# Kernel tuning notes

Hardware: AMD Instinct MI355X
Metric: run time of the kernel (lower is better)

Reference implementation:

```python
import jax, jax.numpy as jnp
import numpy as np

KNN = 8
T = 0.07
EPS = 1e-7

def l2norm(x):
    return x / jnp.sqrt(jnp.sum(x * x, axis=1, keepdims=True))

def nce_softmax_loss(x):
    # CrossEntropyLoss with all labels == 0
    return jnp.mean(jax.nn.logsumexp(x, axis=1) - x[:, 0])

def knn_indices(logits, k):
    # cos_distance_softmax on a single 'sample' [N, C]
    soft = jax.nn.softmax(logits, axis=-1)                      # [N, C]
    w = jnp.linalg.norm(soft, axis=-1)                          # [N]
    sim = (soft @ soft.T) / jnp.clip(w[:, None] * w[None, :], EPS)
    dist = 1.0 - sim
    eye = jnp.eye(logits.shape[0], dtype=dist.dtype)
    dist = dist * (1.0 - eye) - eye                             # diag -> -1 so self is always picked
    _, nbr = jax.lax.top_k(-dist, k)                            # k smallest distances
    return nbr                                                   # [N, k]

def gnn_encode(h, nbr, W, b):
    # DGL TAGConv with k=1 on the knn graph. Edges are j->i for j in knn(i),
    # so every node has in-degree KNN and D^-1/2 A D^-1/2 h == mean over knn neighbors.
    agg = jnp.mean(h[nbr], axis=1)                              # [N, C]
    return l2norm(jnp.concatenate([h, agg], axis=1) @ W + b)

def setup_inputs():
    key = jax.random.key(0)
    ks = jax.random.split(key, 16)
    B, S_DIM, T_DIM, C, N_DATA, K, NCLS = 256, 1024, 2048, 128, 200000, 4096, 100
    stdv = 1.0 / np.sqrt(C / 3.0)
    return {
        "epoch": 1,
        "f_s": jax.random.normal(ks[0], (B, S_DIM), jnp.float32),
        "l_s": jax.random.normal(ks[1], (B, NCLS), jnp.float32),
        "f_t": jax.random.normal(ks[2], (B, T_DIM), jnp.float32),
        "l_t": jax.random.normal(ks[3], (B, NCLS), jnp.float32),
        "idx": jax.random.randint(ks[4], (B,), 0, N_DATA, jnp.int32),
        "contrast_idx": jax.random.randint(ks[5], (B, K), 0, N_DATA, jnp.int32),
        "W_es": jax.random.normal(ks[6], (C, S_DIM), jnp.float32) / np.sqrt(S_DIM),
        "b_es": jnp.zeros((C,), jnp.float32),
        "W_et": jax.random.normal(ks[7], (C, T_DIM), jnp.float32) / np.sqrt(T_DIM),
        "b_et": jnp.zeros((C,), jnp.float32),
        "W_gs": jax.random.normal(ks[8], (2 * C, C), jnp.float32) / np.sqrt(2 * C),
        "b_gs": jnp.zeros((C,), jnp.float32),
        "W_gt": jax.random.normal(ks[9], (2 * C, C), jnp.float32) / np.sqrt(2 * C),
        "b_gt": jnp.zeros((C,), jnp.float32),
        "memory_l": jax.random.uniform(ks[10], (N_DATA, C), jnp.float32, -stdv, stdv),
        "memory_ab": jax.random.uniform(ks[11], (N_DATA, C), jnp.float32, -stdv, stdv),
    }

def reference(epoch, f_s, l_s, f_t, l_t, idx, contrast_idx,
              W_es, b_es, W_et, b_et, W_gs, b_gs, W_gt, b_gt,
              memory_l, memory_ab):
    mem_l = jax.lax.stop_gradient(memory_l)
    mem_ab = jax.lax.stop_gradient(memory_ab)

    # Embed + L2 normalize
    f_es = l2norm(f_s @ W_es.T + b_es)                          # [B, C]
    f_et = l2norm(f_t @ W_et.T + b_et)                          # [B, C]

    # NCEAverage.forward: gather negatives from memory banks
    weight_t = mem_l[contrast_idx]                              # [B, K, C]
    weight_s = mem_ab[contrast_idx]                             # [B, K, C]
    # get_pos
    f_us = mem_l[idx]                                           # [B, C]
    f_ut = mem_ab[idx]                                          # [B, C]

    ls_pos = jnp.sum(f_ut * f_es, axis=1, keepdims=True)        # [B, 1]
    lt_pos = jnp.sum(f_us * f_et, axis=1, keepdims=True)
    ls_neg = jnp.einsum('bkc,bc->bk', weight_t, f_es)           # [B, K]
    lt_neg = jnp.einsum('bkc,bc->bk', weight_s, f_et)
    out_s = jnp.concatenate([ls_pos, ls_neg], axis=1) / T
    out_t = jnp.concatenate([lt_pos, lt_neg], axis=1) / T
    loss = nce_softmax_loss(out_s) + nce_softmax_loss(out_t)

    # GNN branch (batchSize >= knn)
    nbr_s = knn_indices(jax.lax.stop_gradient(l_s), KNN)
    f_gs = gnn_encode(f_es, nbr_s, W_gs, b_gs)                  # [B, C]
    nbr_t = knn_indices(jax.lax.stop_gradient(l_t), KNN)
    f_gt = gnn_encode(f_et, nbr_t, W_gt, b_gt)

    # get_smooth (fully detached, momentum 0.75)
    f_sgs = jax.lax.stop_gradient(l2norm(mem_l[idx] * 0.75 + f_gs * 0.25))
    f_sgt = jax.lax.stop_gradient(l2norm(mem_ab[idx] * 0.75 + f_gt * 0.25))

    gs_pos = jnp.sum(f_sgt * f_gs, axis=1, keepdims=True)
    gt_pos = jnp.sum(f_sgs * f_gt, axis=1, keepdims=True)
    gs_neg = jnp.einsum('bkc,bc->bk', weight_t, f_gs)
    gt_neg = jnp.einsum('bkc,bc->bk', weight_s, f_gt)
    out_gs = jnp.concatenate([gs_pos, gs_neg], axis=1) / T
    out_gt = jnp.concatenate([gt_pos, gt_neg], axis=1) / T
    loss_g = nce_softmax_loss(out_gs) + nce_softmax_loss(out_gt)

    # NOTE: contrast.update() is a no-grad buffer mutation with no effect on the
    # returned loss; omitted from the pure-functional reference.
    return loss + loss_g
```

## Files before the change

### kernel.cpp

```cpp
#include <hip/hip_runtime.h>
#include <math.h>

#define B 256
#define SDIM 1024
#define TDIM 2048
#define C 128
#define NCLS 100
#define KNEG 4096
#define KNN_K 8
#define NCHUNK 16
#define KC (KNEG / NCHUNK)
#define TINV (1.0f / 0.07f)

__global__ __launch_bounds__(256) void embed2_kernel(
    const float* __restrict__ Xs, const float* __restrict__ Ws,
    const float* __restrict__ bs, const float* __restrict__ Xt,
    const float* __restrict__ Wt, const float* __restrict__ bt,
    float* __restrict__ out_s, float* __restrict__ out_t) {
  const int which = blockIdx.y;
  const int S = which ? TDIM : SDIM;
  const float* __restrict__ X = which ? Xt : Xs;
  const float* __restrict__ W = which ? Wt : Ws;
  const float* __restrict__ bias = which ? bt : bs;
  float* __restrict__ out = which ? out_t : out_s;

  __shared__ float xrow[TDIM];
  __shared__ float ob[C];
  __shared__ float ssbuf[4];
  const int b = blockIdx.x;
  const int t = threadIdx.x;
  const int wave = t >> 6, lane = t & 63;

  const float4* xg = (const float4*)(X + (size_t)b * S);
  for (int i = t; i < S / 4; i += 256) ((float4*)xrow)[i] = xg[i];
  __syncthreads();

  const int nj = S / 256;
  for (int ci = 0; ci < 32; ++ci) {
    const int c = wave * 32 + ci;
    const float4* wrow = (const float4*)(W + (size_t)c * S);
    float acc = 0.f;
    for (int j = 0; j < nj; ++j) {
      float4 w4 = wrow[lane + 64 * j];
      float4 x4 = ((const float4*)xrow)[lane + 64 * j];
      acc += w4.x * x4.x + w4.y * x4.y + w4.z * x4.z + w4.w * x4.w;
    }
#pragma unroll
    for (int off = 32; off; off >>= 1) acc += __shfl_xor(acc, off, 64);
    if (lane == 0) ob[c] = acc + bias[c];
  }
  __syncthreads();

  const float v = (t < C) ? ob[t] : 0.f;
  float ss = v * v;
#pragma unroll
  for (int off = 32; off; off >>= 1) ss += __shfl_xor(ss, off, 64);
  if (lane == 0) ssbuf[wave] = ss;
  __syncthreads();
  const float tot = ssbuf[0] + ssbuf[1] + ssbuf[2] + ssbuf[3];
  if (t < C) out[(size_t)b * C + t] = v / sqrtf(tot);
}

__global__ __launch_bounds__(128) void knn_soft_kernel(
    const float* __restrict__ Ls, const float* __restrict__ Lt,
    float* __restrict__ soft_s, float* __restrict__ soft_t,
    float* __restrict__ wn_s, float* __restrict__ wn_t) {
  const int which = blockIdx.y;
  const float* L = which ? Lt : Ls;
  float* soft = which ? soft_t : soft_s;
  float* wn = which ? wn_t : wn_s;
  const int b = blockIdx.x;
  const int t = threadIdx.x;
  const int wave = t >> 6, lane = t & 63;
  __shared__ float r2[2];

  const float x = (t < NCLS) ? L[b * NCLS + t] : -INFINITY;
  float m = x;
#pragma unroll
  for (int off = 32; off; off >>= 1) m = fmaxf(m, __shfl_xor(m, off, 64));
  if (lane == 0) r2[wave] = m;
  __syncthreads();
  m = fmaxf(r2[0], r2[1]);
  __syncthreads();

  const float e = (t < NCLS) ? expf(x - m) : 0.f;
  float s = e;
#pragma unroll
  for (int off = 32; off; off >>= 1) s += __shfl_xor(s, off, 64);
  if (lane == 0) r2[wave] = s;
  __syncthreads();
  s = r2[0] + r2[1];
  __syncthreads();

  const float p = e / s;
  if (t < NCLS) soft[b * NCLS + t] = p;

  float q = p * p;
#pragma unroll
  for (int off = 32; off; off >>= 1) q += __shfl_xor(q, off, 64);
  if (lane == 0) r2[wave] = q;
  __syncthreads();
  if (t == 0) wn[b] = sqrtf(r2[0] + r2[1]);
}

__global__ __launch_bounds__(256) void knn_topk_kernel(
    const float* __restrict__ soft_s, const float* __restrict__ wn_s,
    int* __restrict__ nbr_s, const float* __restrict__ soft_t,
    const float* __restrict__ wn_t, int* __restrict__ nbr_t) {
  const int which = blockIdx.y;
  const float* __restrict__ soft = which ? soft_t : soft_s;
  const float* __restrict__ wn = which ? wn_t : wn_s;
  int* __restrict__ nbr = which ? nbr_t : nbr_s;

  const int i = blockIdx.x;
  const int j = threadIdx.x;
  __shared__ float si[NCLS];
  __shared__ float vals[B];
  __shared__ float rv[B];
  __shared__ int ri[B];

  if (j < NCLS) si[j] = soft[i * NCLS + j];
  __syncthreads();

  float dot = 0.f;
  for (int c = 0; c < NCLS; ++c) dot += si[c] * soft[j * NCLS + c];
  const float denom = fmaxf(wn[i] * wn[j], 1e-7f);
  vals[j] = (j == i) ? 1.0f : (dot / denom - 1.0f);
  __syncthreads();

  for (int r = 0; r < KNN_K; ++r) {
    rv[j] = vals[j];
    ri[j] = j;
    __syncthreads();
    for (int s = 128; s; s >>= 1) {
      if (j < s) {
        const float v2 = rv[j + s];
        const int i2 = ri[j + s];
        if (v2 > rv[j] || (v2 == rv[j] && i2 < ri[j])) { rv[j] = v2; ri[j] = i2; }
      }
      __syncthreads();
    }
    if (j == 0) {
      nbr[i * KNN_K + r] = ri[0];
      vals[ri[0]] = -INFINITY;
    }
    __syncthreads();
  }
}

__global__ __launch_bounds__(256) void gnn_pos_kernel(
    const float* __restrict__ f_es, const float* __restrict__ f_et,
    const int* __restrict__ nbr_s, const int* __restrict__ nbr_t,
    const float* __restrict__ W_gs, const float* __restrict__ b_gs,
    const float* __restrict__ W_gt, const float* __restrict__ b_gt,
    const float* __restrict__ mem_l, const float* __restrict__ mem_ab,
    const int* __restrict__ idx, float* __restrict__ f_gs_out,
    float* __restrict__ f_gt_out, float* __restrict__ pos) {
  const int b = blockIdx.x;
  const int t = threadIdx.x;
  const int half = t >> 7;
  const int c = t & 127;
  const int wave = t >> 6, lane = t & 63;

  const float* __restrict__ h = half ? f_et : f_es;
  const int* __restrict__ nbr = half ? nbr_t : nbr_s;
  const float* __restrict__ Wg = half ? W_gt : W_gs;
  const float* __restrict__ bg = half ? b_gt : b_gs;

  __shared__ float hcat[2][2 * C];
  __shared__ float gbuf[2][C];
  __shared__ float red[4];
  __shared__ float r26[2][6];

  float agg = 0.f;
#pragma unroll
  for (int j = 0; j < KNN_K; ++j)
    agg += h[(size_t)nbr[b * KNN_K + j] * C + c];
  hcat[half][c] = h[(size_t)b * C + c];
  hcat[half][C + c] = agg * (1.0f / KNN_K);
  __syncthreads();

  float acc = bg[c];
  for (int k = 0; k < 2 * C; ++k) acc += hcat[half][k] * Wg[k * C + c];

  float ss = acc * acc;
#pragma unroll
  for (int off = 32; off; off >>= 1) ss += __shfl_xor(ss, off, 64);
  if (lane == 0) red[wave] = ss;
  __syncthreads();
  const float g = acc / sqrtf(red[half * 2] + red[half * 2 + 1]);
  gbuf[half][c] = g;
  (half ? f_gt_out : f_gs_out)[(size_t)b * C + c] = g;
  __syncthreads();

  if (half == 0) {
    const int id = idx[b];
    const float ml = mem_l[(size_t)id * C + c];
    const float mab = mem_ab[(size_t)id * C + c];
    const float es = f_es[(size_t)b * C + c];
    const float et = f_et[(size_t)b * C + c];
    const float gs = gbuf[0][c];
    const float gt = gbuf[1][c];
    const float sgs = 0.75f * ml + 0.25f * gs;
    const float sgt = 0.75f * mab + 0.25f * gt;

    float v6[6] = {sgs * sgs, sgt * sgt, mab * es, ml * et, sgt * gs, sgs * gt};
#pragma unroll
    for (int q = 0; q < 6; ++q) {
      float v = v6[q];
#pragma unroll
      for (int off = 32; off; off >>= 1) v += __shfl_xor(v, off, 64);
      if (lane == 0) r26[wave][q] = v;
    }
  }
  __syncthreads();
  if (t == 0) {
    const float ss_gs = r26[0][0] + r26[1][0];
    const float ss_gt = r26[0][1] + r26[1][1];
    pos[0 * B + b] = r26[0][2] + r26[1][2];
    pos[1 * B + b] = r26[0][3] + r26[1][3];
    pos[2 * B + b] = (r26[0][4] + r26[1][4]) / sqrtf(ss_gt);
    pos[3 * B + b] = (r26[0][5] + r26[1][5]) / sqrtf(ss_gs);
  }
}

__global__ __launch_bounds__(256) void neg_partial_kernel(
    const float* __restrict__ mem_l, const float* __restrict__ mem_ab,
    const int* __restrict__ cidx, const float* __restrict__ f_es,
    const float* __restrict__ f_et, const float* __restrict__ f_gs,
    const float* __restrict__ f_gt, float* __restrict__ partial) {
  const int b = blockIdx.x;
  const int chunk = blockIdx.y;
  const int bank = blockIdx.z;
  const float* __restrict__ mem = bank ? mem_ab : mem_l;
  const float* __restrict__ f1 = bank ? f_et : f_es;
  const float* __restrict__ f2 = bank ? f_gt : f_gs;
  const int t = threadIdx.x;
  const int wave = t >> 6, lane = t & 63;
  const int grp = t >> 4;
  const int lig = t & 15;

  __shared__ int rows[KC];
  __shared__ float rbuf[4][2];

  rows[t] = cidx[(size_t)b * KNEG + chunk * KC + t];

  const float4 x1lo = ((const float4*)f1)[b * 32 + lig];
  const float4 x1hi = ((const float4*)f1)[b * 32 + lig + 16];
  const float4 x2lo = ((const float4*)f2)[b * 32 + lig];
  const float4 x2hi = ((const float4*)f2)[b * 32 + lig + 16];
  __syncthreads();

  float s1 = 0.f, s2 = 0.f;
#pragma unroll
  for (int it = 0; it < 16; ++it) {
    const int row = rows[grp * 16 + it];
    const float4* __restrict__ r = (const float4*)(mem + (size_t)row * C);
    const float4 vlo = r[lig];
    const float4 vhi = r[lig + 16];
    float a1 = vlo.x * x1lo.x + vlo.y * x1lo.y + vlo.z * x1lo.z + vlo.w * x1lo.w
             + vhi.x * x1hi.x + vhi.y * x1hi.y + vhi.z * x1hi.z + vhi.w * x1hi.w;
    float a2 = vlo.x * x2lo.x + vlo.y * x2lo.y + vlo.z * x2lo.z + vlo.w * x2lo.w
             + vhi.x * x2hi.x + vhi.y * x2hi.y + vhi.z * x2hi.z + vhi.w * x2hi.w;
#pragma unroll
    for (int off = 8; off; off >>= 1) {
      a1 += __shfl_xor(a1, off, 64);
      a2 += __shfl_xor(a2, off, 64);
    }
    s1 += __expf(a1 * TINV);
    s2 += __expf(a2 * TINV);
  }
  s1 += __shfl_xor(s1, 32, 64);
  s1 += __shfl_xor(s1, 16, 64);
  s2 += __shfl_xor(s2, 32, 64);
  s2 += __shfl_xor(s2, 16, 64);
  if (lane == 0) { rbuf[wave][0] = s1; rbuf[wave][1] = s2; }
  __syncthreads();
  if (t == 0) {
    const float v1 = rbuf[0][0] + rbuf[1][0] + rbuf[2][0] + rbuf[3][0];
    const float v2 = rbuf[0][1] + rbuf[1][1] + rbuf[2][1] + rbuf[3][1];
    partial[((size_t)bank * B + b) * NCHUNK + chunk] = v1;
    partial[((size_t)(bank + 2) * B + b) * NCHUNK + chunk] = v2;
  }
}

__global__ __launch_bounds__(256) void loss_kernel(
    const float* __restrict__ partial, const float* __restrict__ pos,
    float* __restrict__ out) {
  const int b = threadIdx.x;
  const int wave = b >> 6, lane = b & 63;
  __shared__ float rb[4];
  float contrib = 0.f;
#pragma unroll
  for (int l = 0; l < 4; ++l) {
    const float p = pos[l * B + b] * TINV;
    float s = expf(p);
    for (int ch = 0; ch < NCHUNK; ++ch)
      s += partial[((size_t)l * B + b) * NCHUNK + ch];
    contrib += logf(s) - p;
  }
#pragma unroll
  for (int off = 32; off; off >>= 1) contrib += __shfl_xor(contrib, off, 64);
  if (lane == 0) rb[wave] = contrib;
  __syncthreads();
  if (b == 0) out[0] = (rb[0] + rb[1] + rb[2] + rb[3]) * (1.0f / B);
}

extern "C" void kernel_launch(void* const* d_in, const int* in_sizes, int n_in,
                              void* d_out, int out_size, void* d_ws,
                              size_t ws_size, hipStream_t stream) {
  const float* f_s = (const float*)d_in[1];
  const float* l_s = (const float*)d_in[2];
  const float* f_t = (const float*)d_in[3];
  const float* l_t = (const float*)d_in[4];
  const int* idx = (const int*)d_in[5];
  const int* cidx = (const int*)d_in[6];
  const float* W_es = (const float*)d_in[7];
  const float* b_es = (const float*)d_in[8];
  const float* W_et = (const float*)d_in[9];
  const float* b_et = (const float*)d_in[10];
  const float* W_gs = (const float*)d_in[11];
  const float* b_gs = (const float*)d_in[12];
  const float* W_gt = (const float*)d_in[13];
  const float* b_gt = (const float*)d_in[14];
  const float* mem_l = (const float*)d_in[15];
  const float* mem_ab = (const float*)d_in[16];

  char* w = (char*)d_ws;
  float* ws_f_es = (float*)w;    w += B * C * sizeof(float);
  float* ws_f_et = (float*)w;    w += B * C * sizeof(float);
  float* ws_f_gs = (float*)w;    w += B * C * sizeof(float);
  float* ws_f_gt = (float*)w;    w += B * C * sizeof(float);
  float* ws_soft_s = (float*)w;  w += B * NCLS * sizeof(float);
  float* ws_soft_t = (float*)w;  w += B * NCLS * sizeof(float);
  float* ws_wn_s = (float*)w;    w += B * sizeof(float);
  float* ws_wn_t = (float*)w;    w += B * sizeof(float);
  int* ws_nbr_s = (int*)w;       w += B * KNN_K * sizeof(int);
  int* ws_nbr_t = (int*)w;       w += B * KNN_K * sizeof(int);
  float* ws_pos = (float*)w;     w += 4 * B * sizeof(float);
  float* ws_partial = (float*)w; w += 4 * B * NCHUNK * sizeof(float);

  embed2_kernel<<<dim3(B, 2), 256, 0, stream>>>(f_s, W_es, b_es, f_t, W_et,
                                                b_et, ws_f_es, ws_f_et);

  knn_soft_kernel<<<dim3(B, 2), 128, 0, stream>>>(l_s, l_t, ws_soft_s,
                                                  ws_soft_t, ws_wn_s, ws_wn_t);

  knn_topk_kernel<<<dim3(B, 2), 256, 0, stream>>>(ws_soft_s, ws_wn_s, ws_nbr_s,
                                                  ws_soft_t, ws_wn_t, ws_nbr_t);

  gnn_pos_kernel<<<B, 256, 0, stream>>>(ws_f_es, ws_f_et, ws_nbr_s, ws_nbr_t,
                                        W_gs, b_gs, W_gt, b_gt, mem_l, mem_ab,
                                        idx, ws_f_gs, ws_f_gt, ws_pos);

  neg_partial_kernel<<<dim3(B, NCHUNK, 2), 256, 0, stream>>>(
      mem_l, mem_ab, cidx, ws_f_es, ws_f_et, ws_f_gs, ws_f_gt, ws_partial);

  loss_kernel<<<1, 256, 0, stream>>>(ws_partial, ws_pos, (float*)d_out);
}
```

Baseline: 435.4 us.

## Batch four rows per embed block, wave-level top-k, DPP reductions, prefetch negatives

The embed kernel now handles four batch rows per block, so each W row load feeds four dot products. Cross-lane sums use DPP-based reductions. The knn top-k replaces the shared-memory tree reduction, which needed many barriers, with a single-wave shuffle argmax over four values per lane. The negative-scoring kernel software-pipelines the gathered memory-bank rows two at a time. The embed change cuts the grid to 128 blocks and raises shared memory to 32KB, which may reduce occupancy and parallelism.

```diff
diff --git a/kernel.cpp b/kernel.cpp
--- a/kernel.cpp
+++ b/kernel.cpp
@@ -11,6 +11,28 @@
 #define NCHUNK 16
 #define KC (KNEG / NCHUNK)
 #define TINV (1.0f / 0.07f)
+
+template <int CTRL>
+__device__ __forceinline__ float dpp_add(float v) {
+  const int x = __builtin_amdgcn_update_dpp(0, __float_as_int(v), CTRL, 0xF, 0xF, true);
+  return v + __int_as_float(x);
+}
+__device__ __forceinline__ float sum16(float v) {
+  v = dpp_add<0xB1>(v);
+  v = dpp_add<0x4E>(v);
+  v = dpp_add<0x141>(v);
+  v = dpp_add<0x140>(v);
+  return v;
+}
+__device__ __forceinline__ float wave_sum64(float v) {
+  v = sum16(v);
+  v += __shfl_xor(v, 16, 64);
+  v += __shfl_xor(v, 32, 64);
+  return v;
+}
+__device__ __forceinline__ float dot4(float4 a, float4 b) {
+  return a.x * b.x + a.y * b.y + a.z * b.z + a.w * b.w;
+}
 
 __global__ __launch_bounds__(256) void embed2_kernel(
     const float* __restrict__ Xs, const float* __restrict__ Ws,
@@ -24,41 +46,45 @@
   const float* __restrict__ bias = which ? bt : bs;
   float* __restrict__ out = which ? out_t : out_s;
 
-  __shared__ float xrow[TDIM];
-  __shared__ float ob[C];
-  __shared__ float ssbuf[4];
-  const int b = blockIdx.x;
+  __shared__ float xrow[4 * TDIM];
+  __shared__ float ob[4][C];
+  const int b4 = blockIdx.x * 4;
   const int t = threadIdx.x;
   const int wave = t >> 6, lane = t & 63;
 
-  const float4* xg = (const float4*)(X + (size_t)b * S);
-  for (int i = t; i < S / 4; i += 256) ((float4*)xrow)[i] = xg[i];
+  const float4* xg = (const float4*)(X + (size_t)b4 * S);
+  for (int i = t; i < S; i += 256) ((float4*)xrow)[i] = xg[i];
   __syncthreads();
 
   const int nj = S / 256;
+  const int sq = S / 4;
   for (int ci = 0; ci < 32; ++ci) {
     const int c = wave * 32 + ci;
     const float4* wrow = (const float4*)(W + (size_t)c * S);
-    float acc = 0.f;
+    float a0 = 0.f, a1 = 0.f, a2 = 0.f, a3 = 0.f;
     for (int j = 0; j < nj; ++j) {
-      float4 w4 = wrow[lane + 64 * j];
-      float4 x4 = ((const float4*)xrow)[lane + 64 * j];
-      acc += w4.x * x4.x + w4.y * x4.y + w4.z * x4.z + w4.w * x4.w;
-    }
-#pragma unroll
-    for (int off = 32; off; off >>= 1) acc += __shfl_xor(acc, off, 64);
-    if (lane == 0) ob[c] = acc + bias[c];
-  }
-  __syncthreads();
-
-  const float v = (t < C) ? ob[t] : 0.f;
-  float ss = v * v;
-#pragma unroll
-  for (int off = 32; off; off >>= 1) ss += __shfl_xor(ss, off, 64);
-  if (lane == 0) ssbuf[wave] = ss;
-  __syncthreads();
-  const float tot = ssbuf[0] + ssbuf[1] + ssbuf[2] + ssbuf[3];
-  if (t < C) out[(size_t)b * C + t] = v / sqrtf(tot);
+      const float4 w4 = wrow[lane + 64 * j];
+      a0 += dot4(w4, ((const float4*)xrow)[0 * sq + lane + 64 * j]);
+      a1 += dot4(w4, ((const float4*)xrow)[1 * sq + lane + 64 * j]);
+      a2 += dot4(w4, ((const float4*)xrow)[2 * sq + lane + 64 * j]);
+      a3 += dot4(w4, ((const float4*)xrow)[3 * sq + lane + 64 * j]);
+    }
+    a0 = wave_sum64(a0); a1 = wave_sum64(a1);
+    a2 = wave_sum64(a2); a3 = wave_sum64(a3);
+    if (lane == 0) {
+      const float bb = bias[c];
+      ob[0][c] = a0 + bb; ob[1][c] = a1 + bb;
+      ob[2][c] = a2 + bb; ob[3][c] = a3 + bb;
+    }
+  }
+  __syncthreads();
+
+  const float v1 = ob[wave][lane];
+  const float v2 = ob[wave][lane + 64];
+  const float ss = wave_sum64(v1 * v1 + v2 * v2);
+  const float inv = 1.0f / sqrtf(ss);
+  out[(size_t)(b4 + wave) * C + lane] = v1 * inv;
+  out[(size_t)(b4 + wave) * C + lane + 64] = v2 * inv;
 }
 
 __global__ __launch_bounds__(128) void knn_soft_kernel(
@@ -116,35 +142,40 @@
   const int j = threadIdx.x;
   __shared__ float si[NCLS];
   __shared__ float vals[B];
-  __shared__ float rv[B];
-  __shared__ int ri[B];
 
   if (j < NCLS) si[j] = soft[i * NCLS + j];
   __syncthreads();
 
   float dot = 0.f;
-  for (int c = 0; c < NCLS; ++c) dot += si[c] * soft[j * NCLS + c];
+  const float4* sj4 = (const float4*)(soft + j * NCLS);
+#pragma unroll
+  for (int c = 0; c < NCLS / 4; ++c) dot += dot4(((const float4*)si)[c], sj4[c]);
   const float denom = fmaxf(wn[i] * wn[j], 1e-7f);
   vals[j] = (j == i) ? 1.0f : (dot / denom - 1.0f);
   __syncthreads();
 
-  for (int r = 0; r < KNN_K; ++r) {
-    rv[j] = vals[j];
-    ri[j] = j;
-    __syncthreads();
-    for (int s = 128; s; s >>= 1) {
-      if (j < s) {
-        const float v2 = rv[j + s];
-        const int i2 = ri[j + s];
-        if (v2 > rv[j] || (v2 == rv[j] && i2 < ri[j])) { rv[j] = v2; ri[j] = i2; }
+  if (j < 64) {
+    float v0 = vals[j], v1 = vals[j + 64], v2 = vals[j + 128], v3 = vals[j + 192];
+    for (int r = 0; r < KNN_K; ++r) {
+      float bv = v0; int bi = j;
+      if (v1 > bv) { bv = v1; bi = j + 64; }
+      if (v2 > bv) { bv = v2; bi = j + 128; }
+      if (v3 > bv) { bv = v3; bi = j + 192; }
+#pragma unroll
+      for (int off = 1; off < 64; off <<= 1) {
+        const float ov = __shfl_xor(bv, off, 64);
+        const int oi = __shfl_xor(bi, off, 64);
+        if (ov > bv || (ov == bv && oi < bi)) { bv = ov; bi = oi; }
       }
-      __syncthreads();
-    }
-    if (j == 0) {
-      nbr[i * KNN_K + r] = ri[0];
-      vals[ri[0]] = -INFINITY;
-    }
-    __syncthreads();
+      if (j == 0) nbr[i * KNN_K + r] = bi;
+      if (j == (bi & 63)) {
+        const int q = bi >> 6;
+        if (q == 0) v0 = -INFINITY;
+        else if (q == 1) v1 = -INFINITY;
+        else if (q == 2) v2 = -INFINITY;
+        else v3 = -INFINITY;
+      }
+    }
   }
 }
 
@@ -251,24 +282,28 @@
   const float4 x2hi = ((const float4*)f2)[b * 32 + lig + 16];
   __syncthreads();
 
+  const float4* pa = (const float4*)(mem + ((size_t)rows[grp * 16 + 0] << 7));
+  const float4* pb = (const float4*)(mem + ((size_t)rows[grp * 16 + 1] << 7));
+  float4 alo = pa[lig], ahi = pa[lig + 16];
+  float4 blo = pb[lig], bhi = pb[lig + 16];
+
   float s1 = 0.f, s2 = 0.f;
-#pragma unroll
-  for (int it = 0; it < 16; ++it) {
-    const int row = rows[grp * 16 + it];
-    const float4* __restrict__ r = (const float4*)(mem + (size_t)row * C);
-    const float4 vlo = r[lig];
-    const float4 vhi = r[lig + 16];
-    float a1 = vlo.x * x1lo.x + vlo.y * x1lo.y + vlo.z * x1lo.z + vlo.w * x1lo.w
-             + vhi.x * x1hi.x + vhi.y * x1hi.y + vhi.z * x1hi.z + vhi.w * x1hi.w;
-    float a2 = vlo.x * x2lo.x + vlo.y * x2lo.y + vlo.z * x2lo.z + vlo.w * x2lo.w
-             + vhi.x * x2hi.x + vhi.y * x2hi.y + vhi.z * x2hi.z + vhi.w * x2hi.w;
-#pragma unroll
-    for (int off = 8; off; off >>= 1) {
-      a1 += __shfl_xor(a1, off, 64);
-      a2 += __shfl_xor(a2, off, 64);
-    }
-    s1 += __expf(a1 * TINV);
-    s2 += __expf(a2 * TINV);
+  for (int it = 0; it < 16; it += 2) {
+    const float4 calo = alo, cahi = ahi, cblo = blo, cbhi = bhi;
+    if (it + 2 < 16) {
+      const float4* na = (const float4*)(mem + ((size_t)rows[grp * 16 + it + 2] << 7));
+      const float4* nb = (const float4*)(mem + ((size_t)rows[grp * 16 + it + 3] << 7));
+      alo = na[lig]; ahi = na[lig + 16];
+      blo = nb[lig]; bhi = nb[lig + 16];
+    }
+    float d1a = dot4(calo, x1lo) + dot4(cahi, x1hi);
+    float d2a = dot4(calo, x2lo) + dot4(cahi, x2hi);
+    float d1b = dot4(cblo, x1lo) + dot4(cbhi, x1hi);
+    float d2b = dot4(cblo, x2lo) + dot4(cbhi, x2hi);
+    d1a = sum16(d1a); d2a = sum16(d2a);
+    d1b = sum16(d1b); d2b = sum16(d2b);
+    s1 += __expf(d1a * TINV) + __expf(d1b * TINV);
+    s2 += __expf(d2a * TINV) + __expf(d2b * TINV);
   }
   s1 += __shfl_xor(s1, 32, 64);
   s1 += __shfl_xor(s1, 16, 64);
@@ -340,8 +375,8 @@
   float* ws_pos = (float*)w;     w += 4 * B * sizeof(float);
   float* ws_partial = (float*)w; w += 4 * B * NCHUNK * sizeof(float);
 
-  embed2_kernel<<<dim3(B, 2), 256, 0, stream>>>(f_s, W_es, b_es, f_t, W_et,
-                                                b_et, ws_f_es, ws_f_et);
+  embed2_kernel<<<dim3(B / 4, 2), 256, 0, stream>>>(f_s, W_es, b_es, f_t, W_et,
+                                                    b_et, ws_f_es, ws_f_et);
 
   knn_soft_kernel<<<dim3(B, 2), 128, 0, stream>>>(l_s, l_t, ws_soft_s,
                                                   ws_soft_t, ws_wn_s, ws_wn_t);
```

New measurement: 420.2 us. -3.5%, faster.
